# Performance work log

Measured on AMD Instinct MI355X. Metric: run time of the kernel, lower is better.

The kernel has to match this reference:

```python
import jax, jax.numpy as jnp
import numpy as np
from jax import lax

DIM = 192
D_STATE = 16
D_CONV = 4
EXPAND = 2
DT_RANK = 12  # ceil(192/16)
D_INNER = EXPAND * DIM
MLP_HID = int(DIM * 4.0)
B_, T_, H_, W_ = 2, 8, 24, 24


def _mamba_params(key, prefix):
    ks = jax.random.split(key, 6)
    s = 0.02
    return {
        prefix + "_in_proj_w": jax.random.normal(ks[0], (2 * D_INNER, DIM)) * s,
        prefix + "_conv_w": jax.random.normal(ks[1], (D_INNER, D_CONV)) * s,
        prefix + "_conv_b": jnp.zeros((D_INNER,)),
        prefix + "_x_proj_w": jax.random.normal(ks[2], (DT_RANK + 2 * D_STATE, D_INNER)) * s,
        prefix + "_dt_proj_w": jax.random.normal(ks[3], (D_INNER, DT_RANK)) * s,
        prefix + "_dt_proj_b": jax.random.uniform(ks[4], (D_INNER,), minval=-4.0, maxval=-2.0),
        prefix + "_A_log": jnp.log(jnp.broadcast_to(jnp.arange(1, D_STATE + 1, dtype=jnp.float32), (D_INNER, D_STATE))),
        prefix + "_D": jnp.ones((D_INNER,)),
        prefix + "_out_proj_w": jax.random.normal(ks[5], (DIM, D_INNER)) * s,
    }


def setup_inputs() -> dict:
    key = jax.random.key(0)
    ks = jax.random.split(key, 8)
    s = 0.02
    inp = {"x_in": jax.random.normal(ks[0], (B_, T_, DIM, H_, W_), dtype=jnp.float32)}
    inp["norm1_w"] = jnp.ones((DIM,)); inp["norm1_b"] = jnp.zeros((DIM,))
    inp.update(_mamba_params(ks[1], "s"))
    inp.update(_mamba_params(ks[2], "t"))
    inp["fusion_w"] = jax.random.normal(ks[3], (DIM, 2 * DIM)) * s
    inp["fusion_b"] = jnp.zeros((DIM,))
    inp["norm2_w"] = jnp.ones((DIM,)); inp["norm2_b"] = jnp.zeros((DIM,))
    inp["mlp_w1"] = jax.random.normal(ks[4], (MLP_HID, DIM)) * s
    inp["mlp_b1"] = jnp.zeros((MLP_HID,))
    inp["mlp_w2"] = jax.random.normal(ks[5], (DIM, MLP_HID)) * s
    inp["mlp_b2"] = jnp.zeros((DIM,))
    return inp


def _layer_norm(x, w, b, eps=1e-5):
    m = jnp.mean(x, axis=-1, keepdims=True)
    v = jnp.mean(jnp.square(x - m), axis=-1, keepdims=True)
    return (x - m) * lax.rsqrt(v + eps) * w + b


def _selective_scan(u, delta, A, Bm, Cm, Dp):
    # u, delta: [b,L,d]; A: [d,n]; Bm, Cm: [b,L,n]; Dp: [d]
    dA = jnp.exp(delta[..., None] * A)                       # [b,L,d,n]
    dBu = (delta * u)[..., None] * Bm[:, :, None, :]         # [b,L,d,n]

    def step(h, inp):
        dA_t, dBu_t, C_t = inp                               # [b,d,n],[b,d,n],[b,n]
        h = dA_t * h + dBu_t
        y = jnp.einsum('bdn,bn->bd', h, C_t)
        return h, y

    h0 = jnp.zeros((u.shape[0],) + A.shape, dtype=u.dtype)
    xs = (jnp.moveaxis(dA, 1, 0), jnp.moveaxis(dBu, 1, 0), jnp.moveaxis(Cm, 1, 0))
    _, ys = lax.scan(step, h0, xs)                           # [L,b,d]
    return jnp.moveaxis(ys, 0, 1) + u * Dp


def _mamba(x, in_proj_w, conv_w, conv_b, x_proj_w, dt_proj_w, dt_proj_b, A_log, Dp, out_proj_w):
    # x: [b, L, d_model]
    xz = x @ in_proj_w.T                                     # [b,L,2*d_inner]
    xm, z = jnp.split(xz, 2, axis=-1)
    # causal depthwise conv1d (kernel D_CONV, left-padded)
    xc = jnp.pad(xm, ((0, 0), (D_CONV - 1, 0), (0, 0)))
    kernel = conv_w.T[:, None, :]                            # [W=4, I=1, O=d_inner]
    xm = lax.conv_general_dilated(xc, kernel, (1,), 'VALID',
                                  dimension_numbers=('NWC', 'WIO', 'NWC'),
                                  feature_group_count=D_INNER) + conv_b
    xm = jax.nn.silu(xm)
    dbc = xm @ x_proj_w.T                                    # [b,L,dt_rank+2n]
    dt, Bm, Cm = jnp.split(dbc, [DT_RANK, DT_RANK + D_STATE], axis=-1)
    delta = jax.nn.softplus(dt @ dt_proj_w.T + dt_proj_b)    # [b,L,d_inner]
    A = -jnp.exp(A_log)
    y = _selective_scan(xm, delta, A, Bm, Cm, Dp)
    y = y * jax.nn.silu(z)
    return y @ out_proj_w.T


def reference(x_in, norm1_w, norm1_b,
              s_in_proj_w, s_conv_w, s_conv_b, s_x_proj_w, s_dt_proj_w, s_dt_proj_b, s_A_log, s_D, s_out_proj_w,
              t_in_proj_w, t_conv_w, t_conv_b, t_x_proj_w, t_dt_proj_w, t_dt_proj_b, t_A_log, t_D, t_out_proj_w,
              fusion_w, fusion_b, norm2_w, norm2_b, mlp_w1, mlp_b1, mlp_w2, mlp_b2):
    B, T, C, H, W = x_in.shape
    N = H * W
    x = jnp.transpose(x_in, (0, 1, 3, 4, 2)).reshape(B, T, N, C)
    shortcut = x
    xn = _layer_norm(x, norm1_w, norm1_b)
    out_s = _mamba(xn.reshape(B * T, N, C), s_in_proj_w, s_conv_w, s_conv_b, s_x_proj_w,
                   s_dt_proj_w, s_dt_proj_b, s_A_log, s_D, s_out_proj_w).reshape(B, T, N, C)
    x_t = jnp.transpose(xn, (0, 2, 1, 3)).reshape(B * N, T, C)
    out_t = _mamba(x_t, t_in_proj_w, t_conv_w, t_conv_b, t_x_proj_w,
                   t_dt_proj_w, t_dt_proj_b, t_A_log, t_D, t_out_proj_w)
    out_t = jnp.transpose(out_t.reshape(B, N, T, C), (0, 2, 1, 3))
    fused = jnp.concatenate([out_s, out_t], axis=-1)
    x = shortcut + (fused @ fusion_w.T + fusion_b)
    h = _layer_norm(x, norm2_w, norm2_b)
    h = jax.nn.gelu(h @ mlp_w1.T + mlp_b1, approximate=False) @ mlp_w2.T + mlp_b2
    x = x + h
    return jnp.transpose(x.reshape(B, T, H, W, C), (0, 1, 4, 2, 3))
```

## Files before the change

kernel.cpp:

```cpp
#include <hip/hip_runtime.h>
#include <hip/hip_bf16.h>

#define NB 2
#define NT 8
#define NHW 576
#define NC 192
#define DIN 384
#define NSTATE 16
#define MTOK 9216
#define MLPH 768
#define SCH 36
#define CLEN 16
#define NSEQ_S 16
#define L2E 1.44269504088896f
#define LN2 0.69314718055994f

typedef const __hip_bfloat16* bf16p;
typedef __hip_bfloat16 bf16;

typedef __attribute__((ext_vector_type(8))) short frag_ab;
typedef __attribute__((ext_vector_type(4))) float frag_cd;
typedef __attribute__((ext_vector_type(4))) float f32x4;

__device__ __forceinline__ float b2f(__hip_bfloat16 x) { return __bfloat162float(x); }
__device__ __forceinline__ bf16 f2b(float x) { return __float2bfloat16(x); }

__device__ __forceinline__ bool is_f32(const unsigned* __restrict__ n1w) {
    return n1w[0] == 0x3F800000u;
}

__device__ __forceinline__ float ldv(const void* p, long long i, bool f32) {
    return f32 ? ((const float*)p)[i] : b2f(((const bf16*)p)[i]);
}

__device__ __forceinline__ float siluf(float x) { return x / (1.f + expf(-x)); }
__device__ __forceinline__ float softplus_fast(float x) {
    float e = exp2f(-fabsf(x) * L2E);
    return fmaxf(x, 0.f) + log2f(1.f + e) * LN2;
}
__device__ __forceinline__ float geluf(float x) { return 0.5f * x * (1.f + erff(x * 0.7071067811865476f)); }

__device__ __forceinline__ float wave_sum(float v) {
#pragma unroll
    for (int o = 32; o > 0; o >>= 1) v += __shfl_xor(v, o, 64);
    return v;
}

#define INW_N 147456
#define XW_N  16896
#define OW_N  73728
#define FW_N  73728
#define W1_N  147456
#define W2_N  147456
#define EARLY_TOT (2 * INW_N + 2 * XW_N)
#define LATE_TOT  (2 * OW_N + FW_N + W1_N + W2_N)

__global__ __launch_bounds__(256) void wconv_early(const void* inw_s, const void* inw_t,
                                                   const void* xw_s, const void* xw_t,
                                                   bf16* __restrict__ dst,
                                                   const unsigned* __restrict__ n1w) {
    bool f32 = is_f32(n1w);
    int i = blockIdx.x * 256 + threadIdx.x;
    if (i >= EARLY_TOT) return;
    const void* src; int off;
    if (i < INW_N)            { src = inw_s; off = i; }
    else if (i < 2 * INW_N)   { src = inw_t; off = i - INW_N; }
    else if (i < 2 * INW_N + XW_N) { src = xw_s; off = i - 2 * INW_N; }
    else                      { src = xw_t; off = i - 2 * INW_N - XW_N; }
    dst[i] = f2b(ldv(src, off, f32));
}

__global__ __launch_bounds__(256) void wconv_late(const void* ow_s, const void* ow_t,
                                                  const void* fw, const void* w1, const void* w2,
                                                  bf16* __restrict__ dst,
                                                  const unsigned* __restrict__ n1w) {
    bool f32 = is_f32(n1w);
    int i = blockIdx.x * 256 + threadIdx.x;
    if (i >= LATE_TOT) return;
    const void* src; int off;
    if (i < OW_N)                        { src = ow_s; off = i; }
    else if (i < 2 * OW_N)               { src = ow_t; off = i - OW_N; }
    else if (i < 2 * OW_N + FW_N)        { src = fw;   off = i - 2 * OW_N; }
    else if (i < 2 * OW_N + FW_N + W1_N) { src = w1;   off = i - 2 * OW_N - FW_N; }
    else                                 { src = w2;   off = i - 2 * OW_N - FW_N - W1_N; }
    dst[i] = f2b(ldv(src, off, f32));
}

__global__ __launch_bounds__(256) void ln1_kernel(const void* x_in, const void* w, const void* b,
                                                  bf16* __restrict__ xn,
                                                  bf16* __restrict__ xnt,
                                                  bf16* __restrict__ shortcut,
                                                  const unsigned* __restrict__ n1w) {
    bool f32 = is_f32(n1w);
    int bt = blockIdx.x / 9;
    int hw0 = (blockIdx.x % 9) * 64;
    int bb = bt >> 3, tt = bt & 7;
    int t = threadIdx.x, l = t & 63, wv = t >> 6;
    __shared__ bf16 lv[192 * 66];
    __shared__ float psum[4][64], psq[4][64];
    __shared__ float smean[64], srstd[64];
    __shared__ float swl[192], sbl[192];
    for (int i = t; i < 192; i += 256) { swl[i] = ldv(w, i, f32); sbl[i] = ldv(b, i, f32); }
    float s = 0.f, q = 0.f;
#pragma unroll 4
    for (int cg = 0; cg < 48; cg++) {
        int c = wv * 48 + cg;
        float v = ldv(x_in, (long long)(bt * NC + c) * NHW + hw0 + l, f32);
        lv[c * 66 + l] = f2b(v);
        s += v; q += v * v;
    }
    psum[wv][l] = s; psq[wv][l] = q;
    __syncthreads();
    if (t < 64) {
        float ss = psum[0][t] + psum[1][t] + psum[2][t] + psum[3][t];
        float qq = psq[0][t] + psq[1][t] + psq[2][t] + psq[3][t];
        float mean = ss * (1.f / NC);
        float var = qq * (1.f / NC) - mean * mean;
        smean[t] = mean;
        srstd[t] = rsqrtf(var + 1e-5f);
    }
    __syncthreads();
    for (int jj = 0; jj < 64; jj++) {
        if (t < 192) {
            int n = hw0 + jj;
            long long m = (long long)(bt * NHW + n) * NC + t;
            long long mt = ((long long)(bb * NHW + n) * NT + tt) * NC + t;
            bf16 raw = lv[t * 66 + jj];
            float v = b2f(raw);
            bf16 xv = f2b((v - smean[jj]) * srstd[jj] * swl[t] + sbl[t]);
            shortcut[m] = raw;
            xn[m] = xv;
            xnt[mt] = xv;
        }
    }
}

__global__ __launch_bounds__(256) void ln2_kernel(const float* __restrict__ x, const void* w, const void* b,
                                                  bf16* __restrict__ out,
                                                  const unsigned* __restrict__ n1w) {
    bool f32 = is_f32(n1w);
    int m = blockIdx.x * 4 + (threadIdx.x >> 6);
    int lane = threadIdx.x & 63;
    float v[3];
#pragma unroll
    for (int r = 0; r < 3; r++) v[r] = x[(long long)m * NC + lane + r * 64];
    float s = wave_sum(v[0] + v[1] + v[2]);
    float mean = s * (1.f / NC);
    float q = 0.f;
#pragma unroll
    for (int r = 0; r < 3; r++) { float d = v[r] - mean; q += d * d; }
    q = wave_sum(q);
    float rstd = rsqrtf(q * (1.f / NC) + 1e-5f);
#pragma unroll
    for (int r = 0; r < 3; r++) {
        int c = lane + r * 64;
        out[(long long)m * NC + c] = f2b((v[r] - mean) * rstd * ldv(w, c, f32) + ldv(b, c, f32));
    }
}

__device__ __forceinline__ void store_val(float* p, float v) { *p = v; }
__device__ __forceinline__ void store_val(bf16* p, float v) { *p = f2b(v); }
__device__ __forceinline__ float load_val(const float* p) { return *p; }
__device__ __forceinline__ float load_val(const bf16* p) { return b2f(*p); }

__device__ __forceinline__ long long fmode_rowbase(int FMODE, int gm, int N) {
    if (FMODE == 0) return (long long)gm * N;
    if (FMODE == 1) return (long long)gm * 384;
    int b = gm / (NHW * NT);
    int rr = gm % (NHW * NT);
    int n = rr / NT;
    int t = rr % NT;
    int ms = (b * NT + t) * NHW + n;
    return (long long)ms * 384 + 192;
}

#define LDSTR 40
template <int ACT, int FMODE, bool BCHK, typename OutT, typename AddT>
__global__ __launch_bounds__(256) void gemm_mfma(bf16p A, bf16p W, const void* bias,
                                                 const AddT* __restrict__ addsrc,
                                                 OutT* __restrict__ out,
                                                 int M, int N, int K,
                                                 const unsigned* __restrict__ n1w) {
    bool f32 = is_f32(n1w);
    __shared__ bf16 lds_a[128 * LDSTR];
    __shared__ bf16 lds_b[64 * LDSTR];
    int tid = threadIdx.x;
    int m0 = blockIdx.y * 128, n0 = blockIdx.x * 64;
    int wv = tid >> 6;
    int lane = tid & 63;
    int lr = lane & 15;
    int quad = lane >> 4;
    int wm = (wv >> 1) * 64;
    int wn = (wv & 1) * 32;

    frag_cd acc[4][2] = {};

    for (int kc = 0; kc < K; kc += 32) {
#pragma unroll
        for (int p = 0; p < 2; p++) {
            int idx = p * 256 + tid;
            int row = idx >> 2;
            int kcol = (idx & 3) * 8;
            *(uint4*)&lds_a[row * LDSTR + kcol] =
                *(const uint4*)&A[(size_t)(m0 + row) * K + kc + kcol];
        }
        {
            int row = tid >> 2;
            int kcol = (tid & 3) * 8;
            bool ok = !BCHK || (n0 + row) < N;
            uint4 z = {0, 0, 0, 0};
            *(uint4*)&lds_b[row * LDSTR + kcol] =
                ok ? *(const uint4*)&W[(size_t)(n0 + row) * K + kc + kcol] : z;
        }
        __syncthreads();

        frag_ab af[4], bfr[2];
#pragma unroll
        for (int tm = 0; tm < 4; tm++)
            af[tm] = *(const frag_ab*)&lds_a[(wm + tm * 16 + lr) * LDSTR + quad * 8];
#pragma unroll
        for (int tn = 0; tn < 2; tn++)
            bfr[tn] = *(const frag_ab*)&lds_b[(wn + tn * 16 + lr) * LDSTR + quad * 8];
#pragma unroll
        for (int tm = 0; tm < 4; tm++)
#pragma unroll
            for (int tn = 0; tn < 2; tn++)
                acc[tm][tn] = __builtin_amdgcn_mfma_f32_16x16x32_bf16(
                    af[tm], bfr[tn], acc[tm][tn], 0, 0, 0);
        __syncthreads();
    }

#pragma unroll
    for (int tm = 0; tm < 4; tm++) {
#pragma unroll
        for (int r = 0; r < 4; r++) {
            int gm = m0 + wm + tm * 16 + quad * 4 + r;
            long long rowbase = fmode_rowbase(FMODE, gm, N);
#pragma unroll
            for (int tn = 0; tn < 2; tn++) {
                int gn = n0 + wn + tn * 16 + lr;
                if (BCHK && gn >= N) continue;
                float v = acc[tm][tn][r];
                if (bias) v += ldv(bias, gn, f32);
                if (ACT == 1) v = geluf(v);
                if (addsrc) v += load_val(&addsrc[(long long)gm * N + gn]);
                store_val(&out[rowbase + gn], v);
            }
        }
    }
}

template <bool BCHK, int WOFF, typename OutT>
__global__ __launch_bounds__(256) void gemm_dual(bf16p A0, bf16p A1,
                                                 bf16p W0, bf16p W1,
                                                 OutT* __restrict__ out0,
                                                 OutT* __restrict__ out1,
                                                 int M, int N, int K) {
    __shared__ bf16 lds_a[128 * LDSTR];
    __shared__ bf16 lds_b[64 * LDSTR];
    int tid = threadIdx.x;
    bool br0 = blockIdx.y < (unsigned)(M / 128);
    int m0 = (br0 ? blockIdx.y : blockIdx.y - M / 128) * 128;
    int n0 = blockIdx.x * 64;
    bf16p A = br0 ? A0 : A1;
    bf16p W = br0 ? W0 : W1;
    OutT* out = br0 ? out0 : out1;
    int wv = tid >> 6;
    int lane = tid & 63;
    int lr = lane & 15;
    int quad = lane >> 4;
    int wm = (wv >> 1) * 64;
    int wn = (wv & 1) * 32;

    frag_cd acc[4][2] = {};

    for (int kc = 0; kc < K; kc += 32) {
#pragma unroll
        for (int p = 0; p < 2; p++) {
            int idx = p * 256 + tid;
            int row = idx >> 2;
            int kcol = (idx & 3) * 8;
            *(uint4*)&lds_a[row * LDSTR + kcol] =
                *(const uint4*)&A[(size_t)(m0 + row) * K + kc + kcol];
        }
        {
            int row = tid >> 2;
            int kcol = (tid & 3) * 8;
            bool ok = !BCHK || (n0 + row) < N;
            uint4 z = {0, 0, 0, 0};
            *(uint4*)&lds_b[row * LDSTR + kcol] =
                ok ? *(const uint4*)&W[(size_t)(WOFF + n0 + row) * K + kc + kcol] : z;
        }
        __syncthreads();

        frag_ab af[4], bfr[2];
#pragma unroll
        for (int tm = 0; tm < 4; tm++)
            af[tm] = *(const frag_ab*)&lds_a[(wm + tm * 16 + lr) * LDSTR + quad * 8];
#pragma unroll
        for (int tn = 0; tn < 2; tn++)
            bfr[tn] = *(const frag_ab*)&lds_b[(wn + tn * 16 + lr) * LDSTR + quad * 8];
#pragma unroll
        for (int tm = 0; tm < 4; tm++)
#pragma unroll
            for (int tn = 0; tn < 2; tn++)
                acc[tm][tn] = __builtin_amdgcn_mfma_f32_16x16x32_bf16(
                    af[tm], bfr[tn], acc[tm][tn], 0, 0, 0);
        __syncthreads();
    }

#pragma unroll
    for (int tm = 0; tm < 4; tm++) {
#pragma unroll
        for (int r = 0; r < 4; r++) {
            int gm = m0 + wm + tm * 16 + quad * 4 + r;
#pragma unroll
            for (int tn = 0; tn < 2; tn++) {
                int gn = n0 + wn + tn * 16 + lr;
                if (BCHK && gn >= N) continue;
                store_val(&out[(long long)gm * N + gn], acc[tm][tn][r]);
            }
        }
    }
}

__global__ __launch_bounds__(256) void xproj_z_kernel(
    bf16p xms, bf16p xmt, bf16p xw_s, bf16p xw_t,
    float* __restrict__ dbcs, float* __restrict__ dbct,
    bf16p xn, bf16p xnt, bf16p inw_s, bf16p inw_t,
    bf16* __restrict__ zs, bf16* __restrict__ zt) {
    __shared__ bf16 lds_a[128 * LDSTR];
    __shared__ bf16 lds_b[64 * LDSTR];
    int tid = threadIdx.x;
    int wv = tid >> 6;
    int lane = tid & 63;
    int lr = lane & 15;
    int quad = lane >> 4;
    int wm = (wv >> 1) * 64;
    int wn = (wv & 1) * 32;
    frag_cd acc[4][2] = {};

    if (blockIdx.x < 144) {
        bool br0 = blockIdx.x < 72;
        int m0 = (br0 ? blockIdx.x : blockIdx.x - 72) * 128;
        bf16p A = br0 ? xms : xmt;
        bf16p W = br0 ? xw_s : xw_t;
        float* out = br0 ? dbcs : dbct;
        const int N = 44, K = DIN;
        for (int kc = 0; kc < K; kc += 32) {
#pragma unroll
            for (int p = 0; p < 2; p++) {
                int idx = p * 256 + tid;
                int row = idx >> 2;
                int kcol = (idx & 3) * 8;
                *(uint4*)&lds_a[row * LDSTR + kcol] =
                    *(const uint4*)&A[(size_t)(m0 + row) * K + kc + kcol];
            }
            {
                int row = tid >> 2;
                int kcol = (tid & 3) * 8;
                bool ok = row < N;
                uint4 z = {0, 0, 0, 0};
                *(uint4*)&lds_b[row * LDSTR + kcol] =
                    ok ? *(const uint4*)&W[(size_t)row * K + kc + kcol] : z;
            }
            __syncthreads();
            frag_ab af[4], bfr[2];
#pragma unroll
            for (int tm = 0; tm < 4; tm++)
                af[tm] = *(const frag_ab*)&lds_a[(wm + tm * 16 + lr) * LDSTR + quad * 8];
#pragma unroll
            for (int tn = 0; tn < 2; tn++)
                bfr[tn] = *(const frag_ab*)&lds_b[(wn + tn * 16 + lr) * LDSTR + quad * 8];
#pragma unroll
            for (int tm = 0; tm < 4; tm++)
#pragma unroll
                for (int tn = 0; tn < 2; tn++)
                    acc[tm][tn] = __builtin_amdgcn_mfma_f32_16x16x32_bf16(
                        af[tm], bfr[tn], acc[tm][tn], 0, 0, 0);
            __syncthreads();
        }
#pragma unroll
        for (int tm = 0; tm < 4; tm++) {
#pragma unroll
            for (int r = 0; r < 4; r++) {
                int gm = m0 + wm + tm * 16 + quad * 4 + r;
#pragma unroll
                for (int tn = 0; tn < 2; tn++) {
                    int gn = wn + tn * 16 + lr;
                    if (gn >= N) continue;
                    out[(long long)gm * N + gn] = acc[tm][tn][r];
                }
            }
        }
    } else {
        int rel = blockIdx.x - 144;
        bool br0 = rel < 432;
        int r2 = br0 ? rel : rel - 432;
        int n0 = (r2 % 6) * 64;
        int m0 = (r2 / 6) * 128;
        bf16p A = br0 ? xn : xnt;
        bf16p W = br0 ? inw_s : inw_t;
        bf16* out = br0 ? zs : zt;
        const int N = DIN, K = NC;
        for (int kc = 0; kc < K; kc += 32) {
#pragma unroll
            for (int p = 0; p < 2; p++) {
                int idx = p * 256 + tid;
                int row = idx >> 2;
                int kcol = (idx & 3) * 8;
                *(uint4*)&lds_a[row * LDSTR + kcol] =
                    *(const uint4*)&A[(size_t)(m0 + row) * K + kc + kcol];
            }
            {
                int row = tid >> 2;
                int kcol = (tid & 3) * 8;
                *(uint4*)&lds_b[row * LDSTR + kcol] =
                    *(const uint4*)&W[(size_t)(384 + n0 + row) * K + kc + kcol];
            }
            __syncthreads();
            frag_ab af[4], bfr[2];
#pragma unroll
            for (int tm = 0; tm < 4; tm++)
                af[tm] = *(const frag_ab*)&lds_a[(wm + tm * 16 + lr) * LDSTR + quad * 8];
#pragma unroll
            for (int tn = 0; tn < 2; tn++)
                bfr[tn] = *(const frag_ab*)&lds_b[(wn + tn * 16 + lr) * LDSTR + quad * 8];
#pragma unroll
            for (int tm = 0; tm < 4; tm++)
#pragma unroll
                for (int tn = 0; tn < 2; tn++)
                    acc[tm][tn] = __builtin_amdgcn_mfma_f32_16x16x32_bf16(
                        af[tm], bfr[tn], acc[tm][tn], 0, 0, 0);
            __syncthreads();
        }
#pragma unroll
        for (int tm = 0; tm < 4; tm++) {
#pragma unroll
            for (int r = 0; r < 4; r++) {
                int gm = m0 + wm + tm * 16 + quad * 4 + r;
#pragma unroll
                for (int tn = 0; tn < 2; tn++) {
                    int gn = n0 + wn + tn * 16 + lr;
                    out[(long long)gm * N + gn] = f2b(acc[tm][tn][r]);
                }
            }
        }
    }
}

__global__ __launch_bounds__(256) void gemm_outproj_dual(bf16p ys_s, bf16p ys_t,
                                                         bf16p w_s, bf16p w_t,
                                                         bf16* __restrict__ fused) {
    __shared__ bf16 lds_a[128 * LDSTR];
    __shared__ bf16 lds_b[64 * LDSTR];
    int tid = threadIdx.x;
    bool spatial = blockIdx.y < (MTOK / 128);
    int m0 = (spatial ? blockIdx.y : blockIdx.y - MTOK / 128) * 128;
    int n0 = blockIdx.x * 64;
    bf16p A = spatial ? ys_s : ys_t;
    bf16p W = spatial ? w_s : w_t;
    const int K = DIN;
    int wv = tid >> 6;
    int lane = tid & 63;
    int lr = lane & 15;
    int quad = lane >> 4;
    int wm = (wv >> 1) * 64;
    int wn = (wv & 1) * 32;

    frag_cd acc[4][2] = {};

    for (int kc = 0; kc < K; kc += 32) {
#pragma unroll
        for (int p = 0; p < 2; p++) {
            int idx = p * 256 + tid;
            int row = idx >> 2;
            int kcol = (idx & 3) * 8;
            *(uint4*)&lds_a[row * LDSTR + kcol] =
                *(const uint4*)&A[(size_t)(m0 + row) * K + kc + kcol];
        }
        {
            int row = tid >> 2;
            int kcol = (tid & 3) * 8;
            *(uint4*)&lds_b[row * LDSTR + kcol] =
                *(const uint4*)&W[(size_t)(n0 + row) * K + kc + kcol];
        }
        __syncthreads();

        frag_ab af[4], bfr[2];
#pragma unroll
        for (int tm = 0; tm < 4; tm++)
            af[tm] = *(const frag_ab*)&lds_a[(wm + tm * 16 + lr) * LDSTR + quad * 8];
#pragma unroll
        for (int tn = 0; tn < 2; tn++)
            bfr[tn] = *(const frag_ab*)&lds_b[(wn + tn * 16 + lr) * LDSTR + quad * 8];
#pragma unroll
        for (int tm = 0; tm < 4; tm++)
#pragma unroll
            for (int tn = 0; tn < 2; tn++)
                acc[tm][tn] = __builtin_amdgcn_mfma_f32_16x16x32_bf16(
                    af[tm], bfr[tn], acc[tm][tn], 0, 0, 0);
        __syncthreads();
    }

#pragma unroll
    for (int tm = 0; tm < 4; tm++) {
#pragma unroll
        for (int r = 0; r < 4; r++) {
            int gm = m0 + wm + tm * 16 + quad * 4 + r;
            long long rowbase = fmode_rowbase(spatial ? 1 : 2, gm, NC);
#pragma unroll
            for (int tn = 0; tn < 2; tn++) {
                int gn = n0 + wn + tn * 16 + lr;
                fused[rowbase + gn] = f2b(acc[tm][tn][r]);
            }
        }
    }
}

#define TOTEL (MTOK * DIN)
__global__ __launch_bounds__(256) void conv_dual(bf16p xs, const void* cw_s, const void* cb_s,
                                                 bf16p xt, const void* cw_t, const void* cb_t,
                                                 bf16* __restrict__ xm_s,
                                                 bf16* __restrict__ xm_t,
                                                 const unsigned* __restrict__ n1w) {
    bool f32 = is_f32(n1w);
    long long gidx = (long long)blockIdx.x * blockDim.x + threadIdx.x;
    bool sp = gidx < TOTEL;
    long long idx = sp ? gidx : gidx - TOTEL;
    bf16p x = sp ? xs : xt;
    const void* cw = sp ? cw_s : cw_t;
    const void* cb = sp ? cb_s : cb_t;
    bf16* xm = sp ? xm_s : xm_t;
    int L = sp ? NHW : NT;
    int d = (int)(idx % DIN);
    long long rem = idx / DIN;
    int l = (int)(rem % L);
    long long seq = rem / L;
    float s = ldv(cb, d, f32);
#pragma unroll
    for (int k = 0; k < 4; k++) {
        int ll = l - 3 + k;
        if (ll >= 0) s += ldv(cw, d * 4 + k, f32) * b2f(x[(seq * L + ll) * DIN + d]);
    }
    xm[(seq * L + l) * DIN + d] = f2b(siluf(s));
}

__device__ __forceinline__ void pow_tree8(float pw, float base, float* dA) {
    float p2 = pw * pw;
    float p4 = p2 * p2;
    float p3 = p2 * pw;
    float p6 = p4 * p2;
    float p5 = p4 * pw;
    float p7 = p6 * pw;
    float p8 = p4 * p4;
    dA[0] = base * pw; dA[1] = base * p2; dA[2] = base * p3; dA[3] = base * p4;
    dA[4] = base * p5; dA[5] = base * p6; dA[6] = base * p7; dA[7] = base * p8;
}

__global__ __launch_bounds__(256) void scan_front_kernel(
    bf16p xms, const float* __restrict__ dbcs,
    const void* s_dtw, const void* s_dtb, const void* s_alog,
    bf16* __restrict__ hfin, float* __restrict__ dsumb,
    bf16p xmt, const float* __restrict__ dbct, bf16* __restrict__ zyt,
    const void* t_dtw, const void* t_dtb, const void* t_alog, const void* t_dv,
    const unsigned* __restrict__ n1w) {
    bool f32 = is_f32(n1w);
    __shared__ __align__(16) float sdbc[704];
    int tid = threadIdx.x;

    if (blockIdx.x < 1728) {
        int bid = blockIdx.x;
        int part = bid % 3;
        int ch = (bid / 3) % SCH;
        int seq = bid / (3 * SCH);
        int wave = tid >> 6;
        int lane = tid & 63;
        int dl = lane & 31;
        int nh = lane >> 5;
        int d = part * 128 + wave * 32 + dl;
        int nbase = nh * 8;
        int row0 = seq * NHW + ch * CLEN;
        for (int i = tid; i < CLEN * 44; i += 256)
            sdbc[i] = dbcs[(long long)row0 * 44 + i];
        bf16 um[CLEN];
#pragma unroll
        for (int t = 0; t < CLEN; t++)
            um[t] = xms[(long long)(row0 + t) * DIN + d];
        float A2[8], h[8];
#pragma unroll
        for (int j = 0; j < 8; j++) {
            A2[j] = -expf(ldv(s_alog, d * NSTATE + nbase + j, f32)) * L2E;
            h[j] = 0.f;
        }
        bool st = true;
#pragma unroll
        for (int j = 0; j < 8; j++)
            st = st && (fabsf(A2[j] * (-LN2) - (float)(nbase + j + 1)) < 1e-3f);
        float wdt[12];
#pragma unroll
        for (int r = 0; r < 12; r++) wdt[r] = ldv(s_dtw, d * 12 + r, f32);
        float bdt = ldv(s_dtb, d, f32);
        __syncthreads();
        float dvh[8];
#pragma unroll
        for (int k = 0; k < 8; k++) {
            const float* dr = &sdbc[(nbase + k) * 44];
            f32x4 d0 = *(const f32x4*)&dr[0];
            f32x4 d1 = *(const f32x4*)&dr[4];
            f32x4 d2 = *(const f32x4*)&dr[8];
            float s = bdt;
#pragma unroll
            for (int q = 0; q < 4; q++) s += d0[q] * wdt[q];
#pragma unroll
            for (int q = 0; q < 4; q++) s += d1[q] * wdt[4 + q];
#pragma unroll
            for (int q = 0; q < 4; q++) s += d2[q] * wdt[8 + q];
            dvh[k] = softplus_fast(s);
        }
        float dvo[8];
#pragma unroll
        for (int k = 0; k < 8; k++) dvo[k] = __shfl_xor(dvh[k], 32, 64);
        float dsum = 0.f;
#pragma unroll
        for (int t = 0; t < CLEN; t++) {
            float a = (t < 8) ? dvh[t & 7] : dvo[t & 7];
            float b = (t < 8) ? dvo[t & 7] : dvh[t & 7];
            float dv = nh ? b : a;
            dsum += dv;
            float du = dv * b2f(um[t]);
            const float* dr = &sdbc[t * 44 + 12 + nbase];
            f32x4 B0 = *(const f32x4*)&dr[0];
            f32x4 B1 = *(const f32x4*)&dr[4];
            if (st) {
                float pw = exp2f(-dv * L2E);
                float p2 = pw * pw, p4 = p2 * p2;
                float base = nh ? p4 * p4 : 1.f;
                float dA[8];
                pow_tree8(pw, base, dA);
#pragma unroll
                for (int j = 0; j < 8; j++)
                    h[j] = h[j] * dA[j] + du * (j < 4 ? B0[j & 3] : B1[j & 3]);
            } else {
#pragma unroll
                for (int j = 0; j < 8; j++) {
                    float dA = exp2f(dv * A2[j]);
                    h[j] = h[j] * dA + du * (j < 4 ? B0[j & 3] : B1[j & 3]);
                }
            }
        }
        long long base = (((long long)seq * SCH + ch) * DIN + d) * NSTATE + nbase;
        bf16 ho[8];
// ... 139 lines not shown
    long long base = (((long long)seq * SCH + ch) * DIN + d) * NSTATE + nbase;
    bf16 hi8[8];
    *(uint4*)&hi8[0] = *(const uint4*)&hinit[base];
    float A2[8], h[8];
#pragma unroll
    for (int j = 0; j < 8; j++) {
        A2[j] = -expf(ldv(A_log, d * NSTATE + nbase + j, f32)) * L2E;
        h[j] = b2f(hi8[j]);
    }
    bool st = true;
#pragma unroll
    for (int j = 0; j < 8; j++)
        st = st && (fabsf(A2[j] * (-LN2) - (float)(nbase + j + 1)) < 1e-3f);
    float wdt[12];
#pragma unroll
    for (int r = 0; r < 12; r++) wdt[r] = ldv(dtw, d * 12 + r, f32);
    float bdt = ldv(dtb, d, f32);
    float Dd = ldv(Dv, d, f32);
    __syncthreads();
    float dvh[8];
#pragma unroll
    for (int k = 0; k < 8; k++) {
        const float* dr = &sdbc[(nbase + k) * 44];
        f32x4 d0 = *(const f32x4*)&dr[0];
        f32x4 d1 = *(const f32x4*)&dr[4];
        f32x4 d2 = *(const f32x4*)&dr[8];
        float s = bdt;
#pragma unroll
        for (int q = 0; q < 4; q++) s += d0[q] * wdt[q];
#pragma unroll
        for (int q = 0; q < 4; q++) s += d1[q] * wdt[4 + q];
#pragma unroll
        for (int q = 0; q < 4; q++) s += d2[q] * wdt[8 + q];
        dvh[k] = softplus_fast(s);
    }
    float dvo[8];
#pragma unroll
    for (int k = 0; k < 8; k++) dvo[k] = __shfl_xor(dvh[k], 32, 64);
#pragma unroll
    for (int t = 0; t < CLEN; t++) {
        float a = (t < 8) ? dvh[t & 7] : dvo[t & 7];
        float b = (t < 8) ? dvo[t & 7] : dvh[t & 7];
        float dv = nh ? b : a;
        float uv = b2f(um[t]);
        float du = dv * uv;
        const float* drb = &sdbc[t * 44 + 12 + nbase];
        const float* drc = &sdbc[t * 44 + 28 + nbase];
        f32x4 B0 = *(const f32x4*)&drb[0];
        f32x4 B1 = *(const f32x4*)&drb[4];
        f32x4 C0 = *(const f32x4*)&drc[0];
        f32x4 C1 = *(const f32x4*)&drc[4];
        float y = 0.f;
        if (st) {
            float pw = exp2f(-dv * L2E);
            float p2 = pw * pw, p4 = p2 * p2;
            float base0 = nh ? p4 * p4 : 1.f;
            float dA[8];
            pow_tree8(pw, base0, dA);
#pragma unroll
            for (int j = 0; j < 8; j++) {
                h[j] = h[j] * dA[j] + du * (j < 4 ? B0[j & 3] : B1[j & 3]);
                y += h[j] * (j < 4 ? C0[j & 3] : C1[j & 3]);
            }
        } else {
#pragma unroll
            for (int j = 0; j < 8; j++) {
                float dA = exp2f(dv * A2[j]);
                h[j] = h[j] * dA + du * (j < 4 ? B0[j & 3] : B1[j & 3]);
                y += h[j] * (j < 4 ? C0[j & 3] : C1[j & 3]);
            }
        }
        y += __shfl_xor(y, 32, 64);
        if (nh == 0) {
            y += uv * Dd;
            zy[(long long)(row0 + t) * DIN + d] = f2b(y * siluf(b2f(zm[t])));
        }
    }
}

__global__ __launch_bounds__(256) void out_kernel(const float* __restrict__ fin,
                                                  void* __restrict__ out,
                                                  const unsigned* __restrict__ n1w) {
    bool f32 = is_f32(n1w);
    int bt = blockIdx.x / 9;
    int hw0 = (blockIdx.x % 9) * 64;
    int t = threadIdx.x, l = t & 63, wv = t >> 6;
    __shared__ float lf[192 * 67];
    for (int jj = 0; jj < 64; jj++) {
        if (t < 192)
            lf[t * 67 + jj] = fin[(long long)(bt * NHW + hw0 + jj) * NC + t];
    }
    __syncthreads();
#pragma unroll 4
    for (int cg = 0; cg < 48; cg++) {
        int c = wv * 48 + cg;
        float v = lf[c * 67 + l];
        long long o = (long long)(bt * NC + c) * NHW + hw0 + l;
        if (f32) ((float*)out)[o] = v;
        else     ((bf16*)out)[o] = f2b(v);
    }
}

extern "C" void kernel_launch(void* const* d_in, const int* in_sizes, int n_in,
                              void* d_out, int out_size, void* d_ws, size_t ws_size,
                              hipStream_t stream) {
    const void* x_in   = d_in[0];
    const unsigned* n1w = (const unsigned*)d_in[1];
    const void* n1b    = d_in[2];
    const void* s_inw  = d_in[3];
    const void* s_cw   = d_in[4];
    const void* s_cb   = d_in[5];
    const void* s_xw   = d_in[6];
    const void* s_dtw  = d_in[7];
    const void* s_dtb  = d_in[8];
    const void* s_alog = d_in[9];
    const void* s_d    = d_in[10];
    const void* s_ow   = d_in[11];
    const void* t_inw  = d_in[12];
    const void* t_cw   = d_in[13];
    const void* t_cb   = d_in[14];
    const void* t_xw   = d_in[15];
    const void* t_dtw  = d_in[16];
    const void* t_dtb  = d_in[17];
    const void* t_alog = d_in[18];
    const void* t_d    = d_in[19];
    const void* t_ow   = d_in[20];
    const void* fw     = d_in[21];
    const void* fb     = d_in[22];
    const void* n2w    = d_in[23];
    const void* n2b    = d_in[24];
    const void* w1     = d_in[25];
    const void* b1     = d_in[26];
    const void* w2     = d_in[27];
    const void* b2     = d_in[28];

    char* p = (char*)d_ws;
    p += 16;
    bf16* XN    = (bf16*)p; p += (size_t)MTOK * NC * 2;
    bf16* SHORT = (bf16*)p; p += (size_t)MTOK * NC * 2;
    bf16* XNT   = (bf16*)p; p += (size_t)MTOK * NC * 2;
    bf16* S3    = (bf16*)p; p += (size_t)MTOK * 384 * 2;
    bf16* S4A   = (bf16*)p; p += (size_t)MTOK * DIN * 2;
    bf16* S4B   = (bf16*)p; p += (size_t)MTOK * DIN * 2;
    bf16* S5    = (bf16*)p; p += (size_t)MTOK * DIN * 2;
    bf16* S6    = (bf16*)p; p += (size_t)MTOK * DIN * 2;
    float* DBCS = (float*)p; p += (size_t)MTOK * 44 * 4;
    float* S8   = (float*)p; p += (size_t)MTOK * NC * 4;
    bf16*  HFIN  = S3;
    bf16*  FUSED = S3;
    bf16*  XMS   = S5;
    bf16*  XMT   = S6;
    float* FINAL = (float*)S5;
    bf16*  H     = S6;
    bf16*  HMID  = S4A;
    float* DBCT  = S8;
    float* DSUM  = S8 + (size_t)MTOK * 44;
    float* X2    = S8;

    bf16* CW_INW_S = S3;
    bf16* CW_INW_T = S3 + INW_N;
    bf16* CW_XW_S  = S3 + 2 * INW_N;
    bf16* CW_XW_T  = S3 + 2 * INW_N + XW_N;
    bf16* CW_OW_S = XN;
    bf16* CW_OW_T = XN + OW_N;
    bf16* CW_FW   = XN + 2 * OW_N;
    bf16* CW_W1   = XN + 2 * OW_N + FW_N;
    bf16* CW_W2   = XN + 2 * OW_N + FW_N + W1_N;

    wconv_early<<<(EARLY_TOT + 255) / 256, 256, 0, stream>>>(
        s_inw, t_inw, s_xw, t_xw, CW_INW_S, n1w);

    ln1_kernel<<<144, 256, 0, stream>>>(x_in, n1w, n1b, XN, XNT, SHORT, n1w);

    gemm_dual<false, 0, bf16><<<dim3(DIN / 64, 2 * MTOK / 128), 256, 0, stream>>>(
        XN, XNT, CW_INW_S, CW_INW_T, S4A, S4B, MTOK, DIN, NC);

    conv_dual<<<(unsigned)((2LL * TOTEL + 255) / 256), 256, 0, stream>>>(
        S4A, s_cw, s_cb, S4B, t_cw, t_cb, XMS, XMT, n1w);

    xproj_z_kernel<<<1008, 256, 0, stream>>>(
        XMS, XMT, CW_XW_S, CW_XW_T, DBCS, DBCT,
        XN, XNT, CW_INW_S, CW_INW_T, S4A, S4B);

    wconv_late<<<(LATE_TOT + 255) / 256, 256, 0, stream>>>(
        s_ow, t_ow, fw, w1, w2, CW_OW_S, n1w);

    scan_front_kernel<<<3456, 256, 0, stream>>>(
        XMS, DBCS, s_dtw, s_dtb, s_alog, HFIN, DSUM,
        XMT, DBCT, S4B, t_dtw, t_dtb, t_alog, t_d, n1w);

    scan2_kernel<<<NSEQ_S * DIN * NSTATE / 256, 256, 0, stream>>>(HFIN, DSUM, s_alog, n1w);
    scan3_kernel<<<NSEQ_S * SCH * 3, 256, 0, stream>>>(XMS, DBCS, S4A, s_dtw, s_dtb, s_alog, s_d, HFIN, n1w);

    gemm_outproj_dual<<<dim3(NC / 64, 2 * MTOK / 128), 256, 0, stream>>>(
        S4A, S4B, CW_OW_S, CW_OW_T, FUSED);

    gemm_mfma<0, 0, false, float, bf16><<<dim3(NC / 64, MTOK / 128), 256, 0, stream>>>(
        FUSED, CW_FW, fb, SHORT, X2, MTOK, NC, 2 * NC, n1w);

    ln2_kernel<<<MTOK / 4, 256, 0, stream>>>(X2, n2w, n2b, H, n1w);
    gemm_mfma<1, 0, false, bf16, float><<<dim3(MLPH / 64, MTOK / 128), 256, 0, stream>>>(
        H, CW_W1, b1, nullptr, HMID, MTOK, MLPH, NC, n1w);
    gemm_mfma<0, 0, false, float, float><<<dim3(NC / 64, MTOK / 128), 256, 0, stream>>>(
        HMID, CW_W2, b2, X2, FINAL, MTOK, NC, MLPH, n1w);

    out_kernel<<<144, 256, 0, stream>>>(FINAL, d_out, n1w);
}
```

Measured before the change: 416.1 us.

## Fold weight conversions into other kernels, shrink LN/out tiles, deepen GEMM K-step

The separate early and late weight-conversion kernels become extra blocks appended to the ln1 and scan_front launches, which removes two launches and lets the conversion run alongside other work. The ln1 and out kernels now use 16-token tiles instead of 64, giving 576 blocks instead of 144 for better occupancy on a GPU with many CUs. All MFMA GEMM loops move from a K-step of 32 to 64 with a wider LDS stride, halving the number of barrier pairs per tile at the cost of more LDS per block. The ln1 change also narrows the per-thread write pattern for the transposed outputs.

```diff
diff --git a/kernel.cpp b/kernel.cpp
--- a/kernel.cpp
+++ b/kernel.cpp
@@ -54,78 +54,65 @@
 #define W2_N  147456
 #define EARLY_TOT (2 * INW_N + 2 * XW_N)
 #define LATE_TOT  (2 * OW_N + FW_N + W1_N + W2_N)
-
-__global__ __launch_bounds__(256) void wconv_early(const void* inw_s, const void* inw_t,
-                                                   const void* xw_s, const void* xw_t,
-                                                   bf16* __restrict__ dst,
-                                                   const unsigned* __restrict__ n1w) {
-    bool f32 = is_f32(n1w);
-    int i = blockIdx.x * 256 + threadIdx.x;
-    if (i >= EARLY_TOT) return;
-    const void* src; int off;
-    if (i < INW_N)            { src = inw_s; off = i; }
-    else if (i < 2 * INW_N)   { src = inw_t; off = i - INW_N; }
-    else if (i < 2 * INW_N + XW_N) { src = xw_s; off = i - 2 * INW_N; }
-    else                      { src = xw_t; off = i - 2 * INW_N - XW_N; }
-    dst[i] = f2b(ldv(src, off, f32));
-}
-
-__global__ __launch_bounds__(256) void wconv_late(const void* ow_s, const void* ow_t,
-                                                  const void* fw, const void* w1, const void* w2,
-                                                  bf16* __restrict__ dst,
-                                                  const unsigned* __restrict__ n1w) {
-    bool f32 = is_f32(n1w);
-    int i = blockIdx.x * 256 + threadIdx.x;
-    if (i >= LATE_TOT) return;
-    const void* src; int off;
-    if (i < OW_N)                        { src = ow_s; off = i; }
-    else if (i < 2 * OW_N)               { src = ow_t; off = i - OW_N; }
-    else if (i < 2 * OW_N + FW_N)        { src = fw;   off = i - 2 * OW_N; }
-    else if (i < 2 * OW_N + FW_N + W1_N) { src = w1;   off = i - 2 * OW_N - FW_N; }
-    else                                 { src = w2;   off = i - 2 * OW_N - FW_N - W1_N; }
-    dst[i] = f2b(ldv(src, off, f32));
-}
+#define EARLY_BLKS 1284
+#define LATE_BLKS  2016
 
 __global__ __launch_bounds__(256) void ln1_kernel(const void* x_in, const void* w, const void* b,
                                                   bf16* __restrict__ xn,
                                                   bf16* __restrict__ xnt,
                                                   bf16* __restrict__ shortcut,
+                                                  const void* inw_s, const void* inw_t,
+                                                  const void* xw_s, const void* xw_t,
+                                                  bf16* __restrict__ cwe,
                                                   const unsigned* __restrict__ n1w) {
     bool f32 = is_f32(n1w);
-    int bt = blockIdx.x / 9;
-    int hw0 = (blockIdx.x % 9) * 64;
+    if (blockIdx.x >= 576) {
+        int i = (blockIdx.x - 576) * 256 + threadIdx.x;
+        if (i >= EARLY_TOT) return;
+        const void* src; int off;
+        if (i < INW_N)                 { src = inw_s; off = i; }
+        else if (i < 2 * INW_N)        { src = inw_t; off = i - INW_N; }
+        else if (i < 2 * INW_N + XW_N) { src = xw_s;  off = i - 2 * INW_N; }
+        else                           { src = xw_t;  off = i - 2 * INW_N - XW_N; }
+        cwe[i] = f2b(ldv(src, off, f32));
+        return;
+    }
+    int bt = blockIdx.x / 36;
+    int hw0 = (blockIdx.x % 36) * 16;
     int bb = bt >> 3, tt = bt & 7;
-    int t = threadIdx.x, l = t & 63, wv = t >> 6;
-    __shared__ bf16 lv[192 * 66];
-    __shared__ float psum[4][64], psq[4][64];
-    __shared__ float smean[64], srstd[64];
+    int t = threadIdx.x;
+    int g = t >> 4, l = t & 15;
+    __shared__ bf16 lv[192 * 18];
+    __shared__ float psum[16][16], psq[16][16];
+    __shared__ float smean[16], srstd[16];
     __shared__ float swl[192], sbl[192];
     for (int i = t; i < 192; i += 256) { swl[i] = ldv(w, i, f32); sbl[i] = ldv(b, i, f32); }
     float s = 0.f, q = 0.f;
-#pragma unroll 4
-    for (int cg = 0; cg < 48; cg++) {
-        int c = wv * 48 + cg;
+#pragma unroll
+    for (int cg = 0; cg < 12; cg++) {
+        int c = g * 12 + cg;
         float v = ldv(x_in, (long long)(bt * NC + c) * NHW + hw0 + l, f32);
-        lv[c * 66 + l] = f2b(v);
+        lv[c * 18 + l] = f2b(v);
         s += v; q += v * v;
     }
-    psum[wv][l] = s; psq[wv][l] = q;
+    psum[g][l] = s; psq[g][l] = q;
     __syncthreads();
-    if (t < 64) {
-        float ss = psum[0][t] + psum[1][t] + psum[2][t] + psum[3][t];
-        float qq = psq[0][t] + psq[1][t] + psq[2][t] + psq[3][t];
+    if (t < 16) {
+        float ss = 0.f, qq = 0.f;
+#pragma unroll
+        for (int gg = 0; gg < 16; gg++) { ss += psum[gg][t]; qq += psq[gg][t]; }
         float mean = ss * (1.f / NC);
         float var = qq * (1.f / NC) - mean * mean;
         smean[t] = mean;
         srstd[t] = rsqrtf(var + 1e-5f);
     }
     __syncthreads();
-    for (int jj = 0; jj < 64; jj++) {
+    for (int jj = 0; jj < 16; jj++) {
         if (t < 192) {
             int n = hw0 + jj;
             long long m = (long long)(bt * NHW + n) * NC + t;
             long long mt = ((long long)(bb * NHW + n) * NT + tt) * NC + t;
-            bf16 raw = lv[t * 66 + jj];
+            bf16 raw = lv[t * 18 + jj];
             float v = b2f(raw);
             bf16 xv = f2b((v - smean[jj]) * srstd[jj] * swl[t] + sbl[t]);
             shortcut[m] = raw;
@@ -174,7 +161,7 @@
     return (long long)ms * 384 + 192;
 }
 
-#define LDSTR 40
+#define LDSTR 72
 template <int ACT, int FMODE, bool BCHK, typename OutT, typename AddT>
 __global__ __launch_bounds__(256) void gemm_mfma(bf16p A, bf16p W, const void* bias,
                                                  const AddT* __restrict__ addsrc,
@@ -195,18 +182,20 @@
 
     frag_cd acc[4][2] = {};
 
-    for (int kc = 0; kc < K; kc += 32) {
+    for (int kc = 0; kc < K; kc += 64) {
+#pragma unroll
+        for (int p = 0; p < 4; p++) {
+            int idx = p * 256 + tid;
+            int row = idx >> 3;
+            int kcol = (idx & 7) * 8;
+            *(uint4*)&lds_a[row * LDSTR + kcol] =
+                *(const uint4*)&A[(size_t)(m0 + row) * K + kc + kcol];
+        }
 #pragma unroll
         for (int p = 0; p < 2; p++) {
             int idx = p * 256 + tid;
-            int row = idx >> 2;
-            int kcol = (idx & 3) * 8;
-            *(uint4*)&lds_a[row * LDSTR + kcol] =
-                *(const uint4*)&A[(size_t)(m0 + row) * K + kc + kcol];
-        }
-        {
-            int row = tid >> 2;
-            int kcol = (tid & 3) * 8;
+            int row = idx >> 3;
+            int kcol = (idx & 7) * 8;
             bool ok = !BCHK || (n0 + row) < N;
             uint4 z = {0, 0, 0, 0};
             *(uint4*)&lds_b[row * LDSTR + kcol] =
@@ -214,19 +203,22 @@
         }
         __syncthreads();
 
-        frag_ab af[4], bfr[2];
-#pragma unroll
-        for (int tm = 0; tm < 4; tm++)
-            af[tm] = *(const frag_ab*)&lds_a[(wm + tm * 16 + lr) * LDSTR + quad * 8];
-#pragma unroll
-        for (int tn = 0; tn < 2; tn++)
-            bfr[tn] = *(const frag_ab*)&lds_b[(wn + tn * 16 + lr) * LDSTR + quad * 8];
-#pragma unroll
-        for (int tm = 0; tm < 4; tm++)
+#pragma unroll
+        for (int ks = 0; ks < 2; ks++) {
+            frag_ab af[4], bfr[2];
+#pragma unroll
+            for (int tm = 0; tm < 4; tm++)
+                af[tm] = *(const frag_ab*)&lds_a[(wm + tm * 16 + lr) * LDSTR + ks * 32 + quad * 8];
 #pragma unroll
             for (int tn = 0; tn < 2; tn++)
-                acc[tm][tn] = __builtin_amdgcn_mfma_f32_16x16x32_bf16(
-                    af[tm], bfr[tn], acc[tm][tn], 0, 0, 0);
+                bfr[tn] = *(const frag_ab*)&lds_b[(wn + tn * 16 + lr) * LDSTR + ks * 32 + quad * 8];
+#pragma unroll
+            for (int tm = 0; tm < 4; tm++)
+#pragma unroll
+                for (int tn = 0; tn < 2; tn++)
+                    acc[tm][tn] = __builtin_amdgcn_mfma_f32_16x16x32_bf16(
+                        af[tm], bfr[tn], acc[tm][tn], 0, 0, 0);
+        }
         __syncthreads();
     }
 
@@ -274,18 +266,20 @@
 
     frag_cd acc[4][2] = {};
 
-    for (int kc = 0; kc < K; kc += 32) {
+    for (int kc = 0; kc < K; kc += 64) {
+#pragma unroll
+        for (int p = 0; p < 4; p++) {
+            int idx = p * 256 + tid;
+            int row = idx >> 3;
+            int kcol = (idx & 7) * 8;
+            *(uint4*)&lds_a[row * LDSTR + kcol] =
+                *(const uint4*)&A[(size_t)(m0 + row) * K + kc + kcol];
+        }
 #pragma unroll
         for (int p = 0; p < 2; p++) {
             int idx = p * 256 + tid;
-            int row = idx >> 2;
-            int kcol = (idx & 3) * 8;
-            *(uint4*)&lds_a[row * LDSTR + kcol] =
-                *(const uint4*)&A[(size_t)(m0 + row) * K + kc + kcol];
-        }
-        {
-            int row = tid >> 2;
-            int kcol = (tid & 3) * 8;
+            int row = idx >> 3;
+            int kcol = (idx & 7) * 8;
             bool ok = !BCHK || (n0 + row) < N;
             uint4 z = {0, 0, 0, 0};
             *(uint4*)&lds_b[row * LDSTR + kcol] =
@@ -293,19 +287,22 @@
         }
         __syncthreads();
 
-        frag_ab af[4], bfr[2];
-#pragma unroll
-        for (int tm = 0; tm < 4; tm++)
-            af[tm] = *(const frag_ab*)&lds_a[(wm + tm * 16 + lr) * LDSTR + quad * 8];
-#pragma unroll
-        for (int tn = 0; tn < 2; tn++)
-            bfr[tn] = *(const frag_ab*)&lds_b[(wn + tn * 16 + lr) * LDSTR + quad * 8];
-#pragma unroll
-        for (int tm = 0; tm < 4; tm++)
+#pragma unroll
+        for (int ks = 0; ks < 2; ks++) {
+            frag_ab af[4], bfr[2];
+#pragma unroll
+            for (int tm = 0; tm < 4; tm++)
+                af[tm] = *(const frag_ab*)&lds_a[(wm + tm * 16 + lr) * LDSTR + ks * 32 + quad * 8];
 #pragma unroll
             for (int tn = 0; tn < 2; tn++)
-                acc[tm][tn] = __builtin_amdgcn_mfma_f32_16x16x32_bf16(
-                    af[tm], bfr[tn], acc[tm][tn], 0, 0, 0);
+                bfr[tn] = *(const frag_ab*)&lds_b[(wn + tn * 16 + lr) * LDSTR + ks * 32 + quad * 8];
+#pragma unroll
+            for (int tm = 0; tm < 4; tm++)
+#pragma unroll
+                for (int tn = 0; tn < 2; tn++)
+                    acc[tm][tn] = __builtin_amdgcn_mfma_f32_16x16x32_bf16(
+                        af[tm], bfr[tn], acc[tm][tn], 0, 0, 0);
+        }
         __syncthreads();
     }
 
@@ -347,37 +344,42 @@
         bf16p W = br0 ? xw_s : xw_t;
         float* out = br0 ? dbcs : dbct;
         const int N = 44, K = DIN;
-        for (int kc = 0; kc < K; kc += 32) {
+        for (int kc = 0; kc < K; kc += 64) {
+#pragma unroll
+            for (int p = 0; p < 4; p++) {
+                int idx = p * 256 + tid;
+                int row = idx >> 3;
+                int kcol = (idx & 7) * 8;
+                *(uint4*)&lds_a[row * LDSTR + kcol] =
+                    *(const uint4*)&A[(size_t)(m0 + row) * K + kc + kcol];
+            }
 #pragma unroll
             for (int p = 0; p < 2; p++) {
                 int idx = p * 256 + tid;
-                int row = idx >> 2;
-                int kcol = (idx & 3) * 8;
-                *(uint4*)&lds_a[row * LDSTR + kcol] =
-                    *(const uint4*)&A[(size_t)(m0 + row) * K + kc + kcol];
-            }
-            {
-                int row = tid >> 2;
-                int kcol = (tid & 3) * 8;
+                int row = idx >> 3;
+                int kcol = (idx & 7) * 8;
                 bool ok = row < N;
                 uint4 z = {0, 0, 0, 0};
                 *(uint4*)&lds_b[row * LDSTR + kcol] =
                     ok ? *(const uint4*)&W[(size_t)row * K + kc + kcol] : z;
             }
             __syncthreads();
-            frag_ab af[4], bfr[2];
-#pragma unroll
-            for (int tm = 0; tm < 4; tm++)
-                af[tm] = *(const frag_ab*)&lds_a[(wm + tm * 16 + lr) * LDSTR + quad * 8];
-#pragma unroll
-            for (int tn = 0; tn < 2; tn++)
-                bfr[tn] = *(const frag_ab*)&lds_b[(wn + tn * 16 + lr) * LDSTR + quad * 8];
-#pragma unroll
-            for (int tm = 0; tm < 4; tm++)
+#pragma unroll
+            for (int ks = 0; ks < 2; ks++) {
+                frag_ab af[4], bfr[2];
+#pragma unroll
+                for (int tm = 0; tm < 4; tm++)
+                    af[tm] = *(const frag_ab*)&lds_a[(wm + tm * 16 + lr) * LDSTR + ks * 32 + quad * 8];
 #pragma unroll
                 for (int tn = 0; tn < 2; tn++)
-                    acc[tm][tn] = __builtin_amdgcn_mfma_f32_16x16x32_bf16(
-                        af[tm], bfr[tn], acc[tm][tn], 0, 0, 0);
+                    bfr[tn] = *(const frag_ab*)&lds_b[(wn + tn * 16 + lr) * LDSTR + ks * 32 + quad * 8];
+#pragma unroll
+                for (int tm = 0; tm < 4; tm++)
+#pragma unroll
+                    for (int tn = 0; tn < 2; tn++)
+                        acc[tm][tn] = __builtin_amdgcn_mfma_f32_16x16x32_bf16(
+                            af[tm], bfr[tn], acc[tm][tn], 0, 0, 0);
+            }
             __syncthreads();
         }
 #pragma unroll
@@ -403,35 +405,40 @@
         bf16p W = br0 ? inw_s : inw_t;
         bf16* out = br0 ? zs : zt;
         const int N = DIN, K = NC;
-        for (int kc = 0; kc < K; kc += 32) {
+        for (int kc = 0; kc < K; kc += 64) {
+#pragma unroll
+            for (int p = 0; p < 4; p++) {
+                int idx = p * 256 + tid;
+                int row = idx >> 3;
+                int kcol = (idx & 7) * 8;
+                *(uint4*)&lds_a[row * LDSTR + kcol] =
+                    *(const uint4*)&A[(size_t)(m0 + row) * K + kc + kcol];
+            }
 #pragma unroll
             for (int p = 0; p < 2; p++) {
                 int idx = p * 256 + tid;
-                int row = idx >> 2;
-                int kcol = (idx & 3) * 8;
-                *(uint4*)&lds_a[row * LDSTR + kcol] =
-                    *(const uint4*)&A[(size_t)(m0 + row) * K + kc + kcol];
-            }
-            {
-                int row = tid >> 2;
-                int kcol = (tid & 3) * 8;
+                int row = idx >> 3;
+                int kcol = (idx & 7) * 8;
                 *(uint4*)&lds_b[row * LDSTR + kcol] =
                     *(const uint4*)&W[(size_t)(384 + n0 + row) * K + kc + kcol];
             }
             __syncthreads();
-            frag_ab af[4], bfr[2];
-#pragma unroll
-            for (int tm = 0; tm < 4; tm++)
-                af[tm] = *(const frag_ab*)&lds_a[(wm + tm * 16 + lr) * LDSTR + quad * 8];
-#pragma unroll
-            for (int tn = 0; tn < 2; tn++)
-                bfr[tn] = *(const frag_ab*)&lds_b[(wn + tn * 16 + lr) * LDSTR + quad * 8];
-#pragma unroll
-            for (int tm = 0; tm < 4; tm++)
+#pragma unroll
+            for (int ks = 0; ks < 2; ks++) {
+                frag_ab af[4], bfr[2];
+#pragma unroll
+                for (int tm = 0; tm < 4; tm++)
+                    af[tm] = *(const frag_ab*)&lds_a[(wm + tm * 16 + lr) * LDSTR + ks * 32 + quad * 8];
 #pragma unroll
                 for (int tn = 0; tn < 2; tn++)
-                    acc[tm][tn] = __builtin_amdgcn_mfma_f32_16x16x32_bf16(
-                        af[tm], bfr[tn], acc[tm][tn], 0, 0, 0);
+                    bfr[tn] = *(const frag_ab*)&lds_b[(wn + tn * 16 + lr) * LDSTR + ks * 32 + quad * 8];
+#pragma unroll
+                for (int tm = 0; tm < 4; tm++)
+#pragma unroll
+                    for (int tn = 0; tn < 2; tn++)
+                        acc[tm][tn] = __builtin_amdgcn_mfma_f32_16x16x32_bf16(
+                            af[tm], bfr[tn], acc[tm][tn], 0, 0, 0);
+            }
             __syncthreads();
         }
 #pragma unroll
@@ -470,36 +477,41 @@
 
     frag_cd acc[4][2] = {};
 
-    for (int kc = 0; kc < K; kc += 32) {
+    for (int kc = 0; kc < K; kc += 64) {
+#pragma unroll
+        for (int p = 0; p < 4; p++) {
+            int idx = p * 256 + tid;
+            int row = idx >> 3;
+            int kcol = (idx & 7) * 8;
+            *(uint4*)&lds_a[row * LDSTR + kcol] =
+                *(const uint4*)&A[(size_t)(m0 + row) * K + kc + kcol];
+        }
 #pragma unroll
         for (int p = 0; p < 2; p++) {
             int idx = p * 256 + tid;
-            int row = idx >> 2;
-            int kcol = (idx & 3) * 8;
-            *(uint4*)&lds_a[row * LDSTR + kcol] =
-                *(const uint4*)&A[(size_t)(m0 + row) * K + kc + kcol];
-        }
-        {
-            int row = tid >> 2;
-            int kcol = (tid & 3) * 8;
+            int row = idx >> 3;
+            int kcol = (idx & 7) * 8;
             *(uint4*)&lds_b[row * LDSTR + kcol] =
                 *(const uint4*)&W[(size_t)(n0 + row) * K + kc + kcol];
         }
         __syncthreads();
 
-        frag_ab af[4], bfr[2];
-#pragma unroll
-        for (int tm = 0; tm < 4; tm++)
-            af[tm] = *(const frag_ab*)&lds_a[(wm + tm * 16 + lr) * LDSTR + quad * 8];
-#pragma unroll
-        for (int tn = 0; tn < 2; tn++)
-            bfr[tn] = *(const frag_ab*)&lds_b[(wn + tn * 16 + lr) * LDSTR + quad * 8];
-#pragma unroll
-        for (int tm = 0; tm < 4; tm++)
+#pragma unroll
+        for (int ks = 0; ks < 2; ks++) {
+            frag_ab af[4], bfr[2];
+#pragma unroll
+            for (int tm = 0; tm < 4; tm++)
+                af[tm] = *(const frag_ab*)&lds_a[(wm + tm * 16 + lr) * LDSTR + ks * 32 + quad * 8];
 #pragma unroll
             for (int tn = 0; tn < 2; tn++)
-                acc[tm][tn] = __builtin_amdgcn_mfma_f32_16x16x32_bf16(
-                    af[tm], bfr[tn], acc[tm][tn], 0, 0, 0);
+                bfr[tn] = *(const frag_ab*)&lds_b[(wn + tn * 16 + lr) * LDSTR + ks * 32 + quad * 8];
+#pragma unroll
+            for (int tm = 0; tm < 4; tm++)
+#pragma unroll
+                for (int tn = 0; tn < 2; tn++)
+                    acc[tm][tn] = __builtin_amdgcn_mfma_f32_16x16x32_bf16(
+                        af[tm], bfr[tn], acc[tm][tn], 0, 0, 0);
+        }
         __syncthreads();
     }
 
@@ -564,10 +576,25 @@
     bf16* __restrict__ hfin, float* __restrict__ dsumb,
     bf16p xmt, const float* __restrict__ dbct, bf16* __restrict__ zyt,
     const void* t_dtw, const void* t_dtb, const void* t_alog, const void* t_dv,
+    const void* owx_s, const void* owx_t, const void* fwx,
+    const void* w1x, const void* w2x, bf16* __restrict__ cwl,
     const unsigned* __restrict__ n1w) {
     bool f32 = is_f32(n1w);
     __shared__ __align__(16) float sdbc[704];
     int tid = threadIdx.x;
+
+    if (blockIdx.x >= 3456) {
+        int i = (blockIdx.x - 3456) * 256 + tid;
+        if (i >= LATE_TOT) return;
+        const void* src; int off;
+        if (i < OW_N)                        { src = owx_s; off = i; }
+        else if (i < 2 * OW_N)               { src = owx_t; off = i - OW_N; }
+        else if (i < 2 * OW_N + FW_N)        { src = fwx;   off = i - 2 * OW_N; }
+        else if (i < 2 * OW_N + FW_N + W1_N) { src = w1x;   off = i - 2 * OW_N - FW_N; }
+        else                                 { src = w2x;   off = i - 2 * OW_N - FW_N - W1_N; }
+        cwl[i] = f2b(ldv(src, off, f32));
+        return;
+    }
 
     if (blockIdx.x < 1728) {
         int bid = blockIdx.x;
@@ -873,19 +900,20 @@
                                                   void* __restrict__ out,
                                                   const unsigned* __restrict__ n1w) {
     bool f32 = is_f32(n1w);
-    int bt = blockIdx.x / 9;
-    int hw0 = (blockIdx.x % 9) * 64;
-    int t = threadIdx.x, l = t & 63, wv = t >> 6;
-    __shared__ float lf[192 * 67];
-    for (int jj = 0; jj < 64; jj++) {
+    int bt = blockIdx.x / 36;
+    int hw0 = (blockIdx.x % 36) * 16;
+    int t = threadIdx.x;
+    __shared__ float lf[192 * 17];
+    for (int jj = 0; jj < 16; jj++) {
         if (t < 192)
-            lf[t * 67 + jj] = fin[(long long)(bt * NHW + hw0 + jj) * NC + t];
+            lf[t * 17 + jj] = fin[(long long)(bt * NHW + hw0 + jj) * NC + t];
     }
     __syncthreads();
-#pragma unroll 4
-    for (int cg = 0; cg < 48; cg++) {
-        int c = wv * 48 + cg;
-        float v = lf[c * 67 + l];
+    int g = t >> 4, l = t & 15;
+#pragma unroll
+    for (int cg = 0; cg < 12; cg++) {
+        int c = g * 12 + cg;
+        float v = lf[c * 17 + l];
         long long o = (long long)(bt * NC + c) * NHW + hw0 + l;
         if (f32) ((float*)out)[o] = v;
         else     ((bf16*)out)[o] = f2b(v);
@@ -958,10 +986,8 @@
     bf16* CW_W1   = XN + 2 * OW_N + FW_N;
     bf16* CW_W2   = XN + 2 * OW_N + FW_N + W1_N;
 
-    wconv_early<<<(EARLY_TOT + 255) / 256, 256, 0, stream>>>(
-        s_inw, t_inw, s_xw, t_xw, CW_INW_S, n1w);
-
-    ln1_kernel<<<144, 256, 0, stream>>>(x_in, n1w, n1b, XN, XNT, SHORT, n1w);
+    ln1_kernel<<<576 + EARLY_BLKS, 256, 0, stream>>>(
+        x_in, n1w, n1b, XN, XNT, SHORT, s_inw, t_inw, s_xw, t_xw, CW_INW_S, n1w);
 
     gemm_dual<false, 0, bf16><<<dim3(DIN / 64, 2 * MTOK / 128), 256, 0, stream>>>(
         XN, XNT, CW_INW_S, CW_INW_T, S4A, S4B, MTOK, DIN, NC);
@@ -973,12 +999,10 @@
         XMS, XMT, CW_XW_S, CW_XW_T, DBCS, DBCT,
         XN, XNT, CW_INW_S, CW_INW_T, S4A, S4B);
 
-    wconv_late<<<(LATE_TOT + 255) / 256, 256, 0, stream>>>(
+    scan_front_kernel<<<3456 + LATE_BLKS, 256, 0, stream>>>(
+        XMS, DBCS, s_dtw, s_dtb, s_alog, HFIN, DSUM,
+        XMT, DBCT, S4B, t_dtw, t_dtb, t_alog, t_d,
         s_ow, t_ow, fw, w1, w2, CW_OW_S, n1w);
-
-    scan_front_kernel<<<3456, 256, 0, stream>>>(
-        XMS, DBCS, s_dtw, s_dtb, s_alog, HFIN, DSUM,
-        XMT, DBCT, S4B, t_dtw, t_dtb, t_alog, t_d, n1w);
 
     scan2_kernel<<<NSEQ_S * DIN * NSTATE / 256, 256, 0, stream>>>(HFIN, DSUM, s_alog, n1w);
     scan3_kernel<<<NSEQ_S * SCH * 3, 256, 0, stream>>>(XMS, DBCS, S4A, s_dtw, s_dtb, s_alog, s_d, HFIN, n1w);
@@ -995,5 +1019,5 @@
     gemm_mfma<0, 0, false, float, float><<<dim3(NC / 64, MTOK / 128), 256, 0, stream>>>(
         HMID, CW_W2, b2, X2, FINAL, MTOK, NC, MLPH, n1w);
 
-    out_kernel<<<144, 256, 0, stream>>>(FINAL, d_out, n1w);
-}
+    out_kernel<<<576, 256, 0, stream>>>(FINAL, d_out, n1w);
+}
```

Measured after the change: 384.0 us. 1.08x faster.
